# Kernel optimization log

Measured on AMD Instinct MI355X. Metric: run time of the kernel, lower is better.

## Reference

```python
import jax, jax.numpy as jnp
import numpy as np

# Standard genetic code: 64 codons ordered by bases T,C,A,G (first/second/third position).
AA64 = "FFLLSSSSYY**CC*WLLLLPPPPHHQQRRRRIIIMTTTTNNKKSSRRVVVVAAAADDEEGGGG"
NC = 65  # codon vocab: id 0 = PAD, ids 1..64 = codons
_uniq = sorted(set(AA64))
_gid = {a: i + 1 for i, a in enumerate(_uniq)}          # group 0 reserved for PAD
NG = len(_uniq) + 1                                      # number of AA groups (+dummy)
GROUP_IDS = jnp.asarray(np.array([0] + [_gid[a] for a in AA64], dtype=np.int32))
IS_CODING = jnp.asarray(np.array([False] + [a != '*' for a in AA64]))
_syn = {a: AA64.count(a) for a in _uniq}
NSYN = jnp.asarray(np.array([0.0] + [float(_syn[a]) for a in AA64], dtype=np.float32))

LOSS_W = dict(ce=1.0, cai=0.4, rscu=0.3, gc=0.1, structure=0.15, dynamics=0.1)
EPS = 1e-8


def _cai(codon_ids, species_ids, mask, weight_matrix):
    # per-token gather of CAI weights: [B, L]
    w = weight_matrix[species_ids[:, None], codon_ids]
    log_w = jnp.log(jnp.maximum(w, EPS))
    m = mask.astype(log_w.dtype)
    mean_log = (log_w * m).sum(1) / jnp.maximum(m.sum(1), 1.0)
    return jnp.exp(mean_log)  # [B]


def _seq_rscu(codon_ids, aa_ids, mask):
    # grouped codon histogram -> RSCU: count * n_syn(aa) / total_count(aa)
    B = codon_ids.shape[0]
    bi = jnp.arange(B)[:, None]
    valid = mask & (codon_ids > 0)
    counts = jnp.zeros((B, NC), jnp.float32).at[bi, codon_ids].add(valid.astype(jnp.float32))
    aa_valid = valid & (aa_ids > 2)  # positions with a real amino-acid token
    observed = jnp.zeros((B, NC), jnp.float32).at[bi, codon_ids].add(aa_valid.astype(jnp.float32)) > 0
    observed = observed & IS_CODING[None, :]
    obs_counts = counts * observed  # counts of codons observed under a valid AA
    # segment-sum over synonymous-codon groups
    group_sum = jnp.zeros((B, NG), jnp.float32).at[:, GROUP_IDS].add(obs_counts)
    tot = group_sum[:, GROUP_IDS]  # [B, NC] total count of each codon's syn group
    return jnp.where(observed & (tot > 0), obs_counts * NSYN[None, :] / jnp.maximum(tot, 1.0), 0.0)


def _rscu_kl(pred_ids, target_ids, aa_ids, species_ids, mask, ref_distributions):
    pred_rscu = _seq_rscu(pred_ids, aa_ids, mask)
    target_rscu = _seq_rscu(target_ids, aa_ids, mask)
    ref_rscu = ref_distributions[species_ids]  # [B, NC]
    combined = 0.7 * target_rscu + 0.3 * ref_rscu + EPS
    pred = pred_rscu + EPS
    p = pred / pred.sum(1, keepdims=True)
    t = combined / combined.sum(1, keepdims=True)
    return (t * (jnp.log(t) - jnp.log(p))).sum(1)  # [B]


def setup_inputs() -> dict:
    key = jax.random.key(0)
    ks = jax.random.split(key, 9)
    B, L = 64, 8192
    return {
        "logits": jax.random.normal(ks[0], (B, L, NC), jnp.float32),
        "weight_matrix": jax.random.uniform(ks[1], (5, NC), jnp.float32),
        "ref_distributions": jax.random.uniform(ks[2], (5, NC), jnp.float32) * 2.0,
        "gc_pred": jax.random.uniform(ks[3], (B, L), jnp.float32),
        "mfe": jax.random.normal(ks[4], (B,), jnp.float32) * 5.0 - 20.0,
        "pause_prob": jax.random.uniform(ks[5], (B, L), jnp.float32),
        "target_codon_ids": jax.random.randint(ks[6], (B, L), 0, NC),
        "aa_ids": jax.random.randint(ks[7], (B, L), 0, 25),
        "species_ids": jax.random.randint(ks[8], (B,), 0, 5),
        "mask": jnp.ones((B, L), dtype=bool),
    }


def reference(logits, weight_matrix, ref_distributions, gc_pred, mfe, pause_prob,
              target_codon_ids, aa_ids, species_ids, mask):
    # CE with ignore_index=0
    logp = jax.nn.log_softmax(logits, axis=-1)
    nll = -jnp.take_along_axis(logp, target_codon_ids[..., None], axis=-1)[..., 0]
    v = (target_codon_ids != 0).astype(logits.dtype)
    ce = (nll * v).sum() / jnp.maximum(v.sum(), 1.0)

    pred_ids = jnp.argmax(logits, axis=-1)

    pred_cai = _cai(pred_ids, species_ids, mask, weight_matrix)
    target_cai = _cai(target_codon_ids, species_ids, mask, weight_matrix)
    cai_loss = jax.nn.relu(target_cai - pred_cai).mean()

    rscu_loss = _rscu_kl(pred_ids, target_codon_ids, aa_ids, species_ids, mask, ref_distributions).mean()

    gc_loss = jnp.mean((gc_pred.mean(1) - 0.5) ** 2)
    structure_loss = jnp.mean((mfe - (-20.0)) ** 2)
    dynamics_loss = jnp.mean((pause_prob.mean(1) - 0.1) ** 2)

    total = (LOSS_W['ce'] * ce + LOSS_W['cai'] * cai_loss + LOSS_W['rscu'] * rscu_loss
             + LOSS_W['gc'] * gc_loss + LOSS_W['structure'] * structure_loss
             + LOSS_W['dynamics'] * dynamics_loss)
    return total
```

## Files before the change

kernel.cpp:

```cpp
#include <hip/hip_runtime.h>
#include <math.h>
#include <stdint.h>

#define NCC 65
#define NGG 22
#define BB  64
#define LL  8192
#define EPSF 1e-8f
#define TPB 64
#define PPB 64
#define TILES 4
#define SUBS 32
#define NBLK (BB * SUBS)

__device__ __constant__ int c_gid[NCC] = {0,
  6,6,11,11,17,17,17,17,21,21,1,1,3,3,1,20,
  11,11,11,11,14,14,14,14,8,8,15,15,16,16,16,16,
  9,9,9,12,18,18,18,18,13,13,10,10,17,17,16,16,
  19,19,19,19,2,2,2,2,4,4,5,5,7,7,7,7};
__device__ __constant__ int c_coding[NCC] = {0,
  1,1,1,1,1,1,1,1,1,1,0,0,1,1,0,1,
  1,1,1,1,1,1,1,1,1,1,1,1,1,1,1,1,
  1,1,1,1,1,1,1,1,1,1,1,1,1,1,1,1,
  1,1,1,1,1,1,1,1,1,1,1,1,1,1,1,1};
__device__ __constant__ float c_nsyn[NCC] = {0.f,
  2,2,6,6,6,6,6,6,2,2,3,3,2,2,3,1,
  6,6,6,6,4,4,4,4,2,2,2,2,6,6,6,6,
  3,3,3,1,4,4,4,4,2,2,2,2,6,6,6,6,
  4,4,4,4,4,4,4,4,2,2,2,2,4,4,4,4};

#define WS_NLL  0
#define WS_VC   64
#define WS_LWP  128
#define WS_LWT  192
#define WS_G    256
#define WS_P    320
#define WS_HIST_BYTES 1792

__global__ __launch_bounds__(TPB) void k_main(
    const float* __restrict__ logits, const float* __restrict__ wmat,
    const float* __restrict__ gcp,    const float* __restrict__ ppr,
    const int* __restrict__ tgt,      const int* __restrict__ aa,
    const int* __restrict__ spec,     float* __restrict__ ws)
{
  const int blk = blockIdx.x;
  const int b   = blk >> 5;
  const int tid = threadIdx.x;

  __shared__ float tile[PPB * NCC];
  __shared__ float lwrow[NCC];
  __shared__ int   sh[4 * NCC];

  const int sp = spec[b];
  lwrow[tid] = logf(fmaxf(wmat[sp * NCC + tid], EPSF));
  if (tid == 0) lwrow[64] = logf(fmaxf(wmat[sp * NCC + 64], EPSF));
  #pragma unroll
  for (int i = tid; i < 4 * NCC; i += TPB) sh[i] = 0;

  float nll = 0.f, vc = 0.f, lwp = 0.f, lwt = 0.f, g = 0.f, p = 0.f;

  const int posB0 = (blk & 31) * (TILES * PPB);
  const size_t rowBase = (size_t)b * LL + posB0;

  float4 pf[17];
  {
    const float4* src = (const float4*)(logits + rowBase * NCC);
    #pragma unroll
    for (int j = 0; j < 16; j++) pf[j] = src[j * 64 + tid];
    if (tid < 16) pf[16] = src[1024 + tid];
  }

  for (int tl = 0; tl < TILES; tl++) {
    __syncthreads();
    {
      float4* dst = (float4*)tile;
      #pragma unroll
      for (int j = 0; j < 16; j++) dst[j * 64 + tid] = pf[j];
      if (tid < 16) dst[1024 + tid] = pf[16];
    }
    __syncthreads();

    if (tl + 1 < TILES) {
      const float4* src = (const float4*)(logits + (rowBase + (tl + 1) * PPB) * NCC);
      #pragma unroll
      for (int j = 0; j < 16; j++) pf[j] = src[j * 64 + tid];
      if (tid < 16) pf[16] = src[1024 + tid];
    }

    const size_t gpos = rowBase + tl * PPB + tid;
    g += gcp[gpos];
    p += ppr[gpos];
    const int t = tgt[gpos];
    const int qa = aa[gpos];
    const int base = tid * NCC;

    float r[NCC];
    #pragma unroll
    for (int c = 0; c < NCC; c++) r[c] = tile[base + c];

    float m = r[0]; int am = 0;
    #pragma unroll
    for (int c = 1; c < NCC; c++) {
      if (r[c] > m) { m = r[c]; am = c; }
    }
    float s0 = 0.f, s1 = 0.f, s2 = 0.f, s3 = 0.f;
    #pragma unroll
    for (int c = 0; c < 64; c += 4) {
      s0 += __expf(r[c]     - m);
      s1 += __expf(r[c + 1] - m);
      s2 += __expf(r[c + 2] - m);
      s3 += __expf(r[c + 3] - m);
    }
    float s = (s0 + s1) + (s2 + s3) + __expf(r[64] - m);
    float lse = m + __logf(s);
    float xt  = tile[base + t];

    if (t != 0) {
      nll += lse - xt; vc += 1.f;
      atomicAdd(&sh[130 + t], 1);
      if (qa > 2) atomicAdd(&sh[195 + t], 1);
    }
    if (am != 0) {
      atomicAdd(&sh[am], 1);
      if (qa > 2) atomicAdd(&sh[65 + am], 1);
    }
    lwt += lwrow[t];
    lwp += lwrow[am];
  }

  #pragma unroll
  for (int off = 32; off; off >>= 1) {
    nll += __shfl_xor(nll, off);
    vc  += __shfl_xor(vc,  off);
    lwp += __shfl_xor(lwp, off);
    lwt += __shfl_xor(lwt, off);
    g   += __shfl_xor(g,   off);
    p   += __shfl_xor(p,   off);
  }
  if (tid == 0) {
    atomicAdd(&ws[WS_NLL + b], nll);
    atomicAdd(&ws[WS_VC  + b], vc);
    atomicAdd(&ws[WS_LWP + b], lwp);
    atomicAdd(&ws[WS_LWT + b], lwt);
    atomicAdd(&ws[WS_G   + b], g);
    atomicAdd(&ws[WS_P   + b], p);
  }

  __syncthreads();
  unsigned short* P = (unsigned short*)((char*)ws + WS_HIST_BYTES)
                    + (size_t)blk * 260;
  #pragma unroll
  for (int i = tid; i < 4 * NCC; i += TPB) P[i] = (unsigned short)sh[i];
}

__global__ __launch_bounds__(64) void k_final(
    const float* __restrict__ refd, const float* __restrict__ mfe,
    const int* __restrict__ spec,   const float* __restrict__ ws,
    float* __restrict__ out)
{
  const int b = blockIdx.x;
  const int lane = threadIdx.x;
  const int sp = spec[b];

  __shared__ int sH[4 * NCC];
  __shared__ float gsP[NGG], gsT[NGG];
  if (lane < NGG) { gsP[lane] = 0.f; gsT[lane] = 0.f; }

  const unsigned short* P = (const unsigned short*)((const char*)ws + WS_HIST_BYTES);
  for (int idx = lane; idx < 4 * NCC; idx += 64) {
    int s = 0;
    #pragma unroll
    for (int k = 0; k < SUBS; k++)
      s += P[(size_t)(b * SUBS + k) * 260 + idx];
    sH[idx] = s;
  }
  __syncthreads();

  const int   cs[2]  = {lane, 64};
  const bool  act[2] = {true, lane == 0};
  float ocP[2], ocT[2];
  int   obP[2], obT[2];

  #pragma unroll
  for (int k = 0; k < 2; k++) {
    ocP[k] = 0.f; ocT[k] = 0.f; obP[k] = 0; obT[k] = 0;
    if (act[k]) {
      const int c = cs[k];
      int hv = sH[          c];
      int ha = sH[    NCC + c];
      obP[k] = (ha > 0) && c_coding[c];
      ocP[k] = obP[k] ? (float)hv : 0.f;
      if (ocP[k] != 0.f) atomicAdd(&gsP[c_gid[c]], ocP[k]);
      hv = sH[2 * NCC + c];
      ha = sH[3 * NCC + c];
      obT[k] = (ha > 0) && c_coding[c];
      ocT[k] = obT[k] ? (float)hv : 0.f;
      if (ocT[k] != 0.f) atomicAdd(&gsT[c_gid[c]], ocT[k]);
    }
  }
  __syncthreads();

  float pv[2], tv[2];
  float psum = 0.f, tsum = 0.f;
  #pragma unroll
  for (int k = 0; k < 2; k++) {
    pv[k] = 0.f; tv[k] = 0.f;
    if (act[k]) {
      const int c = cs[k];
      float totP = gsP[c_gid[c]];
      float rP = (obP[k] && totP > 0.f) ? ocP[k] * c_nsyn[c] / fmaxf(totP, 1.f) : 0.f;
      float totT = gsT[c_gid[c]];
      float rT = (obT[k] && totT > 0.f) ? ocT[k] * c_nsyn[c] / fmaxf(totT, 1.f) : 0.f;
      pv[k] = rP + EPSF;
      tv[k] = 0.7f * rT + 0.3f * refd[sp * NCC + c] + EPSF;
      psum += pv[k]; tsum += tv[k];
    }
  }
  #pragma unroll
  for (int off = 32; off; off >>= 1) {
    psum += __shfl_xor(psum, off);
    tsum += __shfl_xor(tsum, off);
  }
  float kl = 0.f;
  #pragma unroll
  for (int k = 0; k < 2; k++) {
    if (act[k]) {
      float pn = pv[k] / psum;
      float tn = tv[k] / tsum;
      kl += tn * (logf(tn) - logf(pn));
    }
  }
  #pragma unroll
  for (int off = 32; off; off >>= 1) kl += __shfl_xor(kl, off);

  float part = 0.f;
  if (lane == 0) {
    float pred_cai = expf(ws[WS_LWP + b] * (1.f / (float)LL));
    float tgt_cai  = expf(ws[WS_LWT + b] * (1.f / (float)LL));
    float cai_t = fmaxf(tgt_cai - pred_cai, 0.f);
    float gc_t = ws[WS_G + b] * (1.f / (float)LL) - 0.5f; gc_t *= gc_t;
    float ps_t = ws[WS_P + b] * (1.f / (float)LL) - 0.1f; ps_t *= ps_t;
    float mf   = mfe[b] + 20.f;
    float mf_t = mf * mf;
    float inv = 1.f / (float)BB;
    part = 0.4f  * cai_t * inv
         + 0.3f  * kl    * inv
         + 0.1f  * gc_t  * inv
         + 0.15f * mf_t  * inv
         + 0.1f  * ps_t  * inv;
  }
  if (b == 0) {
    float n = ws[WS_NLL + lane];
    float v = ws[WS_VC  + lane];
    #pragma unroll
    for (int off = 32; off; off >>= 1) {
      n += __shfl_xor(n, off);
      v += __shfl_xor(v, off);
    }
    if (lane == 0) part += n / fmaxf(v, 1.f);
  }
  if (lane == 0) atomicAdd(out, part);
}

extern "C" void kernel_launch(void* const* d_in, const int* in_sizes, int n_in,
                              void* d_out, int out_size, void* d_ws, size_t ws_size,
                              hipStream_t stream) {
  const float* logits = (const float*)d_in[0];
  const float* wmat   = (const float*)d_in[1];
  const float* refd   = (const float*)d_in[2];
  const float* gcp    = (const float*)d_in[3];
  const float* mfe    = (const float*)d_in[4];
  const float* ppr    = (const float*)d_in[5];
  const int*   tgt    = (const int*)d_in[6];
  const int*   aa     = (const int*)d_in[7];
  const int*   spec   = (const int*)d_in[8];
  float* ws = (float*)d_ws;

  hipMemsetAsync(d_ws, 0, 384 * sizeof(float), stream);
  hipMemsetAsync(d_out, 0, sizeof(float), stream);

  k_main<<<dim3(NBLK), dim3(TPB), 0, stream>>>(logits, wmat, gcp, ppr,
                                               tgt, aa, spec, ws);
  k_final<<<dim3(BB), dim3(64), 0, stream>>>(refd, mfe, spec, ws, (float*)d_out);
}
```

Before: 265.6 us.

## Stream logits tiles directly into double-buffered LDS via global_load_lds

Replaces the register-staged prefetch of each 64x65 logits tile with direct global-to-LDS loads into a double-buffered shared tile. Vmcnt waits order the loads instead of block barriers, and the per-position side inputs (gc, pause, target, aa) are hoisted and loaded up front. The aim is to free the 17 float4 staging registers, drop the LDS store pass and the syncthreads, and overlap the next tile's load with compute. It doubles LDS use, and it depends on vmcnt counting being exact; the count of 17 is wrong for threads with tid>=16, which issue only 16 loads, and there is no barrier for cross-lane LDS visibility since the block is a single wave.

```diff
diff --git a/kernel.cpp b/kernel.cpp
--- a/kernel.cpp
+++ b/kernel.cpp
@@ -12,6 +12,14 @@
 #define TILES 4
 #define SUBS 32
 #define NBLK (BB * SUBS)
+
+#define VMCNT_IMM(n) (((n) & 15) | (7u << 4) | (15u << 8) | ((((unsigned)(n)) >> 4) << 14))
+
+__device__ __forceinline__ void load_lds16(const float* g, float* l) {
+  __builtin_amdgcn_global_load_lds(
+      (const __attribute__((address_space(1))) void*)g,
+      (__attribute__((address_space(3))) void*)l, 16, 0, 0);
+}
 
 __device__ __constant__ int c_gid[NCC] = {0,
   6,6,11,11,17,17,17,17,21,21,1,1,3,3,1,20,
@@ -47,7 +55,7 @@
   const int b   = blk >> 5;
   const int tid = threadIdx.x;
 
-  __shared__ float tile[PPB * NCC];
+  __shared__ float tile[2][PPB * NCC];
   __shared__ float lwrow[NCC];
   __shared__ int   sh[4 * NCC];
 
@@ -57,46 +65,55 @@
   #pragma unroll
   for (int i = tid; i < 4 * NCC; i += TPB) sh[i] = 0;
 
+  const size_t rowBase = (size_t)b * LL + (blk & 31) * (TILES * PPB);
+
+  float g4[TILES], p4[TILES];
+  int   t4[TILES], q4[TILES];
+  #pragma unroll
+  for (int tl = 0; tl < TILES; tl++) {
+    const size_t gpos = rowBase + tl * PPB + tid;
+    g4[tl] = gcp[gpos];
+    p4[tl] = ppr[gpos];
+    t4[tl] = tgt[gpos];
+    q4[tl] = aa[gpos];
+  }
+
+  {
+    const float* src = logits + rowBase * NCC;
+    #pragma unroll
+    for (int j = 0; j < 16; j++)
+      load_lds16(src + (size_t)(j * 64 + tid) * 4, &tile[0][j * 256]);
+    if (tid < 16)
+      load_lds16(src + (size_t)(1024 + tid) * 4, &tile[0][4096]);
+  }
+
   float nll = 0.f, vc = 0.f, lwp = 0.f, lwt = 0.f, g = 0.f, p = 0.f;
 
-  const int posB0 = (blk & 31) * (TILES * PPB);
-  const size_t rowBase = (size_t)b * LL + posB0;
-
-  float4 pf[17];
-  {
-    const float4* src = (const float4*)(logits + rowBase * NCC);
-    #pragma unroll
-    for (int j = 0; j < 16; j++) pf[j] = src[j * 64 + tid];
-    if (tid < 16) pf[16] = src[1024 + tid];
-  }
-
   for (int tl = 0; tl < TILES; tl++) {
-    __syncthreads();
-    {
-      float4* dst = (float4*)tile;
+    if (tl + 1 < TILES) {
+      const float* src = logits + (rowBase + (tl + 1) * PPB) * NCC;
       #pragma unroll
-      for (int j = 0; j < 16; j++) dst[j * 64 + tid] = pf[j];
-      if (tid < 16) dst[1024 + tid] = pf[16];
-    }
-    __syncthreads();
-
-    if (tl + 1 < TILES) {
-      const float4* src = (const float4*)(logits + (rowBase + (tl + 1) * PPB) * NCC);
-      #pragma unroll
-      for (int j = 0; j < 16; j++) pf[j] = src[j * 64 + tid];
-      if (tid < 16) pf[16] = src[1024 + tid];
-    }
-
-    const size_t gpos = rowBase + tl * PPB + tid;
-    g += gcp[gpos];
-    p += ppr[gpos];
-    const int t = tgt[gpos];
-    const int qa = aa[gpos];
+      for (int j = 0; j < 16; j++)
+        load_lds16(src + (size_t)(j * 64 + tid) * 4,
+                   &tile[(tl + 1) & 1][j * 256]);
+      if (tid < 16)
+        load_lds16(src + (size_t)(1024 + tid) * 4, &tile[(tl + 1) & 1][4096]);
+      __builtin_amdgcn_s_waitcnt(VMCNT_IMM(17));
+    } else {
+      __builtin_amdgcn_s_waitcnt(VMCNT_IMM(0));
+    }
+    __builtin_amdgcn_sched_barrier(0);
+
+    const float* tb = tile[tl & 1];
+    const int t  = t4[tl];
+    const int qa = q4[tl];
+    g += g4[tl];
+    p += p4[tl];
     const int base = tid * NCC;
 
     float r[NCC];
     #pragma unroll
-    for (int c = 0; c < NCC; c++) r[c] = tile[base + c];
+    for (int c = 0; c < NCC; c++) r[c] = tb[base + c];
 
     float m = r[0]; int am = 0;
     #pragma unroll
@@ -113,7 +130,7 @@
     }
     float s = (s0 + s1) + (s2 + s3) + __expf(r[64] - m);
     float lse = m + __logf(s);
-    float xt  = tile[base + t];
+    float xt  = tb[base + t];
 
     if (t != 0) {
       nll += lse - xt; vc += 1.f;
```

Result: faster. 231.5 us (-12.8%).
